# Kernel optimization log

Hardware: AMD Instinct MI355X
Metric: run time of the kernel (lower is better)

Reference implementation:

```python
import jax, jax.numpy as jnp
import numpy as np
import math
jax.config.update("jax_enable_x64", True)

# dims matching init_kwargs
BS, N_IND, N_STEP, ORDER = 32, 8, 100, 2
N_ORD = ORDER + 1            # number of derivative orders tracked (y, y', y'')
N_IV, N_IV_STEPS = 2, 1
NVAR = N_STEP * N_ORD        # qp variables per ODE (eps column is dropped: A[..., 1:])
DT = jnp.float64             # solver_dbl=True


def _static_parts():
    # initial-value constraint rows: u[t, j] = iv_rhs for t < n_iv_steps, j < n_iv
    iv_rows = N_IV_STEPS * N_IV
    Iv = np.zeros((iv_rows, NVAR))
    r = 0
    for t in range(N_IV_STEPS):
        for j in range(N_IV):
            Iv[r, t * N_ORD + j] = 1.0
            r += 1
    # Taylor expansion tables: fact[i, j] = 1/(j-i)! for j>=i else 0; expn[i,j] = j-i
    i_idx = np.arange(ORDER)[:, None]
    j_idx = np.arange(N_ORD)[None, :]
    dmask = j_idx >= i_idx
    d = np.where(dmask, j_idx - i_idx, 0)
    fact = np.where(dmask, 1.0 / np.array([[math.factorial(v) for v in row] for row in d]), 0.0)
    sign = np.where(dmask, (-1.0) ** d, 0.0)
    Imat = np.eye(ORDER, N_ORD)
    return (jnp.asarray(Iv, DT), jnp.asarray(fact, DT), jnp.asarray(d, DT),
            jnp.asarray(sign, DT), jnp.asarray(Imat, DT))


def _solve(coeffs, rhs, iv_rhs, steps):
    # coeffs: (B, n_step, n_ord), rhs: (B, n_step), iv_rhs: (B, iv_rows), steps: (B, n_step-1)
    B = coeffs.shape[0]
    T1 = N_STEP - 1
    R = 2 * ORDER + 1  # fwd Taylor rows (ORDER) + bwd Taylor rows (ORDER) + central row (1)
    Iv, fact, expn, sign, Imat = _static_parts()

    # equation constraints: block-diagonal in step: sum_j coeffs[b,t,j] * u[t,j] = rhs[b,t]
    eye = jnp.eye(N_STEP, dtype=DT)
    Eq = jnp.einsum('ts,bsj->btsj', eye, coeffs).reshape(B, N_STEP, NVAR)
    IvB = jnp.broadcast_to(Iv[None], (B,) + Iv.shape)

    # smoothness constraints per interval t -> t+1 with step h = steps[b,t]
    h = steps[:, :, None, None]                  # (B, T1, 1, 1)
    hp = h ** expn                               # h^(j-i)
    fwd_t = fact * hp                            # fwd Taylor: sum_j h^(j-i)/(j-i)! u[t,j] - u[t+1,i] = 0
    bwd_t1 = fact * sign * hp                    # bwd Taylor: sum_j (-h)^(j-i)/(j-i)! u[t+1,j] - u[t,i] = 0
    ImB = jnp.broadcast_to(Imat, fwd_t.shape)
    hh = steps[:, :, None]                       # (B, T1, 1)
    e_m1 = jnp.zeros((N_ORD,), DT).at[ORDER - 1].set(1.0)
    e_o = jnp.zeros((N_ORD,), DT).at[ORDER].set(1.0)
    # central (trapezoid) rule on highest derivative:
    # u[t+1,ord-1] - u[t,ord-1] - h/2 (u[t,ord] + u[t+1,ord]) = 0
    ct = -e_m1 - 0.5 * hh * e_o                  # (B, T1, n_ord) coeffs on block t
    ct1 = e_m1 - 0.5 * hh * e_o                  # coeffs on block t+1
    Dt = jnp.concatenate([fwd_t, -ImB, ct[:, :, None, :]], axis=2)    # (B,T1,R,n_ord)
    Dt1 = jnp.concatenate([-ImB, bwd_t1, ct1[:, :, None, :]], axis=2)

    Dfull = jnp.zeros((B, T1, R, N_STEP, N_ORD), DT)
    t = jnp.arange(T1)
    Dfull = Dfull.at[:, t, :, t, :].set(jnp.moveaxis(Dt, 1, 0))
    Dfull = Dfull.at[:, t, :, t + 1, :].set(jnp.moveaxis(Dt1, 1, 0))
    D = Dfull.reshape(B, T1 * R, NVAR)

    A = jnp.concatenate([Eq, IvB, D], axis=1)    # dense AG (eps column dropped)
    beta = jnp.concatenate([rhs, iv_rhs, jnp.zeros((B, T1 * R), DT)], axis=1)

    AtA = jnp.einsum('bmi,bmj->bij', A, A)
    Atb = jnp.einsum('bmi,bm->bi', A, beta)
    L = jnp.linalg.cholesky(AtA)
    x = jax.scipy.linalg.cho_solve((L, True), Atb[..., None])[..., 0]
    return x


def setup_inputs() -> dict:
    key = jax.random.key(0)
    k1, k2, k3, k4 = jax.random.split(key, 4)
    coeffs = jax.random.normal(k1, (BS, N_IND, N_STEP, N_ORD), dtype=jnp.float32)
    rhs = jax.random.normal(k2, (BS, N_IND, N_STEP), dtype=jnp.float32)
    iv_rhs = jax.random.normal(k3, (BS, N_IND, N_IV_STEPS * N_IV), dtype=jnp.float32)
    # positive step sizes around the module's step_size=0.1
    steps = 0.05 + 0.1 * jax.random.uniform(k4, (BS, N_IND, N_STEP - 1), dtype=jnp.float32)
    return {"coeffs": coeffs, "rhs": rhs, "iv_rhs": iv_rhs, "steps": steps}


def reference(coeffs, rhs, iv_rhs, steps):
    B = BS * N_IND
    c = coeffs.reshape(B, N_STEP, N_ORD).astype(DT)   # n_dim = 1 folded in
    r = rhs.reshape(B, N_STEP).astype(DT)
    iv = iv_rhs.reshape(B, N_IV_STEPS * N_IV).astype(DT)
    st = steps.reshape(B, N_STEP - 1).astype(DT)
    x = _solve(c, r, iv, st)
    u = x.reshape(BS, N_IND, N_STEP, N_ORD)
    u0, u1, u2 = u[..., 0], u[..., 1], u[..., 2]
    eps = jnp.zeros((B,), DT)
    return (u0, u1, u2, eps, st[:, :, None])
```

## Files before the change

### kernel.cpp

```cpp
#include <hip/hip_runtime.h>

#define NPROB 256
#define NSTEP 100
#define T1    99

__device__ __forceinline__ void syminv3(const float A[6], float G[6]) {
    const float k00 = A[3] * A[5] - A[4] * A[4];
    const float k01 = A[2] * A[4] - A[1] * A[5];
    const float k02 = A[1] * A[4] - A[2] * A[3];
    const float det = A[0] * k00 + A[1] * k01 + A[2] * k02;
    const float id  = 1.0f / det;
    G[0] = k00 * id;
    G[1] = k01 * id;
    G[2] = k02 * id;
    G[3] = (A[0] * A[5] - A[2] * A[2]) * id;
    G[4] = (A[2] * A[1] - A[0] * A[4]) * id;
    G[5] = (A[0] * A[3] - A[1] * A[1]) * id;
}

__device__ __forceinline__ void symmul(const float G[6], const float M[9], float R[9]) {
#pragma unroll
    for (int c = 0; c < 3; ++c) {
        R[0 + c] = G[0] * M[c] + G[1] * M[3 + c] + G[2] * M[6 + c];
        R[3 + c] = G[1] * M[c] + G[3] * M[3 + c] + G[4] * M[6 + c];
        R[6 + c] = G[2] * M[c] + G[4] * M[3 + c] + G[5] * M[6 + c];
    }
}

__device__ __forceinline__ void symvec(const float G[6], const float v[3], float r[3]) {
    r[0] = G[0] * v[0] + G[1] * v[1] + G[2] * v[2];
    r[1] = G[1] * v[0] + G[3] * v[1] + G[4] * v[2];
    r[2] = G[2] * v[0] + G[4] * v[1] + G[5] * v[2];
}

__device__ __forceinline__ void pqz(const float A[6], const float C[9],
                                    const float B[9], const float b[3], float pub[21]) {
    float G[6];
    syminv3(A, G);
    symmul(G, C, pub);
    symmul(G, B, pub + 9);
    symvec(G, b, pub + 18);
}

__device__ __forceinline__ void upd(float A[6], float C[9], float B[9], float b[3],
                                    const float SL[21], const float SR[21]) {
    const float* Pl = SL;      const float* Ql = SL + 9;  const float* zl = SL + 18;
    const float* Pr = SR;      const float* Qr = SR + 9;  const float* zr = SR + 18;

    const int RI[6] = {0, 0, 0, 1, 1, 2};
    const int CI[6] = {0, 1, 2, 1, 2, 2};
#pragma unroll
    for (int e = 0; e < 6; ++e) {
        const int r = RI[e], c = CI[e];
        A[e] -= C[3 * r] * Ql[c] + C[3 * r + 1] * Ql[3 + c] + C[3 * r + 2] * Ql[6 + c]
              + B[3 * r] * Pr[c] + B[3 * r + 1] * Pr[3 + c] + B[3 * r + 2] * Pr[6 + c];
    }
    float nC[9], nB[9];
#pragma unroll
    for (int r = 0; r < 3; ++r)
#pragma unroll
        for (int c = 0; c < 3; ++c) {
            nC[3 * r + c] = -(C[3 * r] * Pl[c] + C[3 * r + 1] * Pl[3 + c] + C[3 * r + 2] * Pl[6 + c]);
            nB[3 * r + c] = -(B[3 * r] * Qr[c] + B[3 * r + 1] * Qr[3 + c] + B[3 * r + 2] * Qr[6 + c]);
        }
#pragma unroll
    for (int r = 0; r < 3; ++r)
        b[r] -= C[3 * r] * zl[0] + C[3 * r + 1] * zl[1] + C[3 * r + 2] * zl[2]
              + B[3 * r] * zr[0] + B[3 * r + 1] * zr[1] + B[3 * r + 2] * zr[2];
#pragma unroll
    for (int k = 0; k < 9; ++k) { C[k] = nC[k]; B[k] = nB[k]; }
}

__device__ __forceinline__ void build_row(int t, const float* cb, const float* rb,
                                          const float* sb, const float* ivp,
                                          float A[6], float C[9], float B[9], float b[3]) {
    const float c0 = cb[t * 3 + 0];
    const float c1 = cb[t * 3 + 1];
    const float c2 = cb[t * 3 + 2];
    const float r  = rb[t];
    A[0] = c0 * c0; A[1] = c0 * c1; A[2] = c0 * c2;
    A[3] = c1 * c1; A[4] = c1 * c2; A[5] = c2 * c2;
    b[0] = c0 * r;  b[1] = c1 * r;  b[2] = c2 * r;
#pragma unroll
    for (int k = 0; k < 9; ++k) { C[k] = 0.0f; B[k] = 0.0f; }

    if (t == 0) {
        A[0] += 1.0f; A[3] += 1.0f;
        b[0] += ivp[0];
        b[1] += ivp[1];
    }
    if (t < T1) {
        const float h = sb[t], h2 = h * h;
        A[0] += 2.0f;
        A[1] += h;
        A[2] += 0.5f * h2;
        A[3] += h2 + 3.0f;
        A[4] += 0.5f * h2 * h + 1.5f * h;
        A[5] += 0.25f * h2 * h2 + 1.25f * h2;
        B[0] = -2.0f;      B[1] =  h;        B[2] = -0.5f * h2;
        B[3] = -h;         B[4] = -3.0f;     B[5] =  1.5f * h;
        B[6] = -0.5f * h2; B[7] = -1.5f * h; B[8] =  0.25f * h2;
    }
    if (t > 0) {
        const float hm = sb[t - 1], hm2 = hm * hm;
        A[0] += 2.0f;
        A[1] -= hm;
        A[2] += 0.5f * hm2;
        A[3] += hm2 + 3.0f;
        A[4] -= 0.5f * hm2 * hm + 1.5f * hm;
        A[5] += 0.25f * hm2 * hm2 + 1.25f * hm2;
        C[0] = -2.0f;      C[1] = -hm;       C[2] = -0.5f * hm2;
        C[3] =  hm;        C[4] = -3.0f;     C[5] = -1.5f * hm;
        C[6] = -0.5f * hm2; C[7] = 1.5f * hm; C[8] = 0.25f * hm2;
    }
}

__device__ __forceinline__ void shflup21(const float v[21], float o[21], int s) {
#pragma unroll
    for (int k = 0; k < 21; ++k) o[k] = __shfl_up(v[k], s, 64);
}
__device__ __forceinline__ void shfldn21(const float v[21], float o[21], int s) {
#pragma unroll
    for (int k = 0; k < 21; ++k) o[k] = __shfl_down(v[k], s, 64);
}

__global__ __launch_bounds__(64, 1) void ode_pcr_shfl_kernel(
    const float* __restrict__ coeffs,
    const float* __restrict__ rhs,
    const float* __restrict__ iv_rhs,
    const float* __restrict__ steps,
    float* __restrict__ out)
{
    const int b = blockIdx.x;
    const int L = threadIdx.x;
    const bool act = (L < 50);

    const float* cb  = coeffs + b * NSTEP * 3;
    const float* rb  = rhs    + b * NSTEP;
    const float* sb  = steps  + b * T1;
    const float* ivp = iv_rhs + b * 2;

    float Ae[6], Ce[9], Be[9], be[3];
    float pubo[21];
#pragma unroll
    for (int k = 0; k < 21; ++k) pubo[k] = 0.0f;
#pragma unroll
    for (int k = 0; k < 6; ++k) Ae[k] = 0.0f;
#pragma unroll
    for (int k = 0; k < 9; ++k) { Ce[k] = 0.0f; Be[k] = 0.0f; }
    be[0] = be[1] = be[2] = 0.0f;

    if (act) {
        build_row(2 * L, cb, rb, sb, ivp, Ae, Ce, Be, be);
        float Ao[6], Co[9], Bo[9], bo[3];
        build_row(2 * L + 1, cb, rb, sb, ivp, Ao, Co, Bo, bo);
        pqz(Ao, Co, Bo, bo, pubo);
    }
    {
        float SL[21];
        shflup21(pubo, SL, 1);
        if (act) upd(Ae, Ce, Be, be, SL, pubo);
    }

#pragma unroll
    for (int lv = 0; lv < 6; ++lv) {
        const int s = 1 << lv;
        float pub[21];
#pragma unroll
        for (int k = 0; k < 21; ++k) pub[k] = 0.0f;
        if (act) pqz(Ae, Ce, Be, be, pub);
        float SL[21], SR[21];
        shflup21(pub, SL, s);
        shfldn21(pub, SR, s);
        if (act) upd(Ae, Ce, Be, be, SL, SR);
    }

    float xe[3] = {0.0f, 0.0f, 0.0f};
    if (act) {
        float G[6];
        syminv3(Ae, G);
        symvec(G, be, xe);
    }
    float xr[3];
    xr[0] = __shfl_down(xe[0], 1, 64);
    xr[1] = __shfl_down(xe[1], 1, 64);
    xr[2] = __shfl_down(xe[2], 1, 64);

    if (act) {
        const float* Po = pubo;
        const float* Qo = pubo + 9;
        const float* zo = pubo + 18;
        float xo[3];
#pragma unroll
        for (int r = 0; r < 3; ++r)
            xo[r] = zo[r]
                  - (Po[3 * r] * xe[0] + Po[3 * r + 1] * xe[1] + Po[3 * r + 2] * xe[2])
                  - (Qo[3 * r] * xr[0] + Qo[3 * r + 1] * xr[1] + Qo[3 * r + 2] * xr[2]);

        const int t0 = 2 * L, t1 = 2 * L + 1;
        out[            b * NSTEP + t0] = xe[0];
        out[            b * NSTEP + t1] = xo[0];
        out[25600 +     b * NSTEP + t0] = xe[1];
        out[25600 +     b * NSTEP + t1] = xo[1];
        out[51200 +     b * NSTEP + t0] = xe[2];
        out[51200 +     b * NSTEP + t1] = xo[2];
    }

    for (int t = L; t < T1; t += 64)
        out[77056 + b * T1 + t] = sb[t];
    if (L == 0)
        out[76800 + b] = 0.0f;
}

extern "C" void kernel_launch(void* const* d_in, const int* in_sizes, int n_in,
                              void* d_out, int out_size, void* d_ws, size_t ws_size,
                              hipStream_t stream) {
    const float* coeffs = (const float*)d_in[0];
    const float* rhs    = (const float*)d_in[1];
    const float* iv_rhs = (const float*)d_in[2];
    const float* steps  = (const float*)d_in[3];
    float* out = (float*)d_out;

    ode_pcr_shfl_kernel<<<dim3(NPROB), dim3(64), 0, stream>>>(
        coeffs, rhs, iv_rhs, steps, out);
}
```

Measured before the change: 65.05 us.

## Exploit block-tridiagonal symmetry in PCR to cut shuffles and matmuls

Reformulates the parallel cyclic reduction to use the symmetry of the normal-equation matrix (C = B^T of the previous row). Only the super-diagonal block is kept, and each lane exchanges compact symmetric products (W, y, G, z, Q) with its neighbours instead of full 21-float P/Q/z packets. The Q shuffle and the B update are also skipped on the final level. The goal is fewer cross-lane shuffles and less arithmetic per reduction level, at the cost of more intricate bookkeeping and possible changes in floating-point rounding.

```diff
diff --git a/kernel.cpp b/kernel.cpp
--- a/kernel.cpp
+++ b/kernel.cpp
@@ -27,53 +27,62 @@
     }
 }
 
+__device__ __forceinline__ void mulsym(const float M[9], const float G[6], float R[9]) {
+#pragma unroll
+    for (int r = 0; r < 3; ++r) {
+        R[3 * r + 0] = M[3 * r + 0] * G[0] + M[3 * r + 1] * G[1] + M[3 * r + 2] * G[2];
+        R[3 * r + 1] = M[3 * r + 0] * G[1] + M[3 * r + 1] * G[3] + M[3 * r + 2] * G[4];
+        R[3 * r + 2] = M[3 * r + 0] * G[2] + M[3 * r + 1] * G[4] + M[3 * r + 2] * G[5];
+    }
+}
+
 __device__ __forceinline__ void symvec(const float G[6], const float v[3], float r[3]) {
     r[0] = G[0] * v[0] + G[1] * v[1] + G[2] * v[2];
     r[1] = G[1] * v[0] + G[3] * v[1] + G[4] * v[2];
     r[2] = G[2] * v[0] + G[4] * v[1] + G[5] * v[2];
 }
 
-__device__ __forceinline__ void pqz(const float A[6], const float C[9],
-                                    const float B[9], const float b[3], float pub[21]) {
-    float G[6];
-    syminv3(A, G);
-    symmul(G, C, pub);
-    symmul(G, B, pub + 9);
-    symvec(G, b, pub + 18);
-}
-
-__device__ __forceinline__ void upd(float A[6], float C[9], float B[9], float b[3],
-                                    const float SL[21], const float SR[21]) {
-    const float* Pl = SL;      const float* Ql = SL + 9;  const float* zl = SL + 18;
-    const float* Pr = SR;      const float* Qr = SR + 9;  const float* zr = SR + 18;
-
-    const int RI[6] = {0, 0, 0, 1, 1, 2};
-    const int CI[6] = {0, 1, 2, 1, 2, 2};
-#pragma unroll
-    for (int e = 0; e < 6; ++e) {
-        const int r = RI[e], c = CI[e];
-        A[e] -= C[3 * r] * Ql[c] + C[3 * r + 1] * Ql[3 + c] + C[3 * r + 2] * Ql[6 + c]
-              + B[3 * r] * Pr[c] + B[3 * r + 1] * Pr[3 + c] + B[3 * r + 2] * Pr[6 + c];
-    }
-    float nC[9], nB[9];
+__device__ __forceinline__ void tvec(const float B[9], const float v[3], float r[3]) {
+#pragma unroll
+    for (int c = 0; c < 3; ++c)
+        r[c] = B[c] * v[0] + B[3 + c] * v[1] + B[6 + c] * v[2];
+}
+
+__device__ __forceinline__ void mvec(const float B[9], const float v[3], float r[3]) {
+#pragma unroll
+    for (int rr = 0; rr < 3; ++rr)
+        r[rr] = B[3 * rr] * v[0] + B[3 * rr + 1] * v[1] + B[3 * rr + 2] * v[2];
+}
+
+__device__ __forceinline__ void nmatmul(const float X[9], const float Y[9], float R[9]) {
 #pragma unroll
     for (int r = 0; r < 3; ++r)
 #pragma unroll
-        for (int c = 0; c < 3; ++c) {
-            nC[3 * r + c] = -(C[3 * r] * Pl[c] + C[3 * r + 1] * Pl[3 + c] + C[3 * r + 2] * Pl[6 + c]);
-            nB[3 * r + c] = -(B[3 * r] * Qr[c] + B[3 * r + 1] * Qr[3 + c] + B[3 * r + 2] * Qr[6 + c]);
-        }
-#pragma unroll
-    for (int r = 0; r < 3; ++r)
-        b[r] -= C[3 * r] * zl[0] + C[3 * r + 1] * zl[1] + C[3 * r + 2] * zl[2]
-              + B[3 * r] * zr[0] + B[3 * r + 1] * zr[1] + B[3 * r + 2] * zr[2];
-#pragma unroll
-    for (int k = 0; k < 9; ++k) { C[k] = nC[k]; B[k] = nB[k]; }
-}
-
-__device__ __forceinline__ void build_row(int t, const float* cb, const float* rb,
+        for (int c = 0; c < 3; ++c)
+            R[3 * r + c] = -(X[3 * r] * Y[c] + X[3 * r + 1] * Y[3 + c] + X[3 * r + 2] * Y[6 + c]);
+}
+
+__device__ __forceinline__ void mulbt_sym(const float M[9], const float B[9], float U[6]) {
+    U[0] = M[0] * B[0] + M[1] * B[1] + M[2] * B[2];
+    U[1] = M[0] * B[3] + M[1] * B[4] + M[2] * B[5];
+    U[2] = M[0] * B[6] + M[1] * B[7] + M[2] * B[8];
+    U[3] = M[3] * B[3] + M[4] * B[4] + M[5] * B[5];
+    U[4] = M[3] * B[6] + M[4] * B[7] + M[5] * B[8];
+    U[5] = M[6] * B[6] + M[7] * B[7] + M[8] * B[8];
+}
+
+__device__ __forceinline__ void btq_sym(const float B[9], const float Q[9], float W[6]) {
+    W[0] = B[0] * Q[0] + B[3] * Q[3] + B[6] * Q[6];
+    W[1] = B[0] * Q[1] + B[3] * Q[4] + B[6] * Q[7];
+    W[2] = B[0] * Q[2] + B[3] * Q[5] + B[6] * Q[8];
+    W[3] = B[1] * Q[1] + B[4] * Q[4] + B[7] * Q[7];
+    W[4] = B[1] * Q[2] + B[4] * Q[5] + B[7] * Q[8];
+    W[5] = B[2] * Q[2] + B[5] * Q[5] + B[8] * Q[8];
+}
+
+__device__ __forceinline__ void build_sym(int t, const float* cb, const float* rb,
                                           const float* sb, const float* ivp,
-                                          float A[6], float C[9], float B[9], float b[3]) {
+                                          float A[6], float B[9], float b[3]) {
     const float c0 = cb[t * 3 + 0];
     const float c1 = cb[t * 3 + 1];
     const float c2 = cb[t * 3 + 2];
@@ -82,7 +91,7 @@
     A[3] = c1 * c1; A[4] = c1 * c2; A[5] = c2 * c2;
     b[0] = c0 * r;  b[1] = c1 * r;  b[2] = c2 * r;
 #pragma unroll
-    for (int k = 0; k < 9; ++k) { C[k] = 0.0f; B[k] = 0.0f; }
+    for (int k = 0; k < 9; ++k) B[k] = 0.0f;
 
     if (t == 0) {
         A[0] += 1.0f; A[3] += 1.0f;
@@ -109,22 +118,21 @@
         A[3] += hm2 + 3.0f;
         A[4] -= 0.5f * hm2 * hm + 1.5f * hm;
         A[5] += 0.25f * hm2 * hm2 + 1.25f * hm2;
-        C[0] = -2.0f;      C[1] = -hm;       C[2] = -0.5f * hm2;
-        C[3] =  hm;        C[4] = -3.0f;     C[5] = -1.5f * hm;
-        C[6] = -0.5f * hm2; C[7] = 1.5f * hm; C[8] = 0.25f * hm2;
-    }
-}
-
-__device__ __forceinline__ void shflup21(const float v[21], float o[21], int s) {
-#pragma unroll
-    for (int k = 0; k < 21; ++k) o[k] = __shfl_up(v[k], s, 64);
-}
-__device__ __forceinline__ void shfldn21(const float v[21], float o[21], int s) {
-#pragma unroll
-    for (int k = 0; k < 21; ++k) o[k] = __shfl_down(v[k], s, 64);
-}
-
-__global__ __launch_bounds__(64, 1) void ode_pcr_shfl_kernel(
+    }
+}
+
+template <int N>
+__device__ __forceinline__ void shup(const float* v, float* o, int s) {
+#pragma unroll
+    for (int k = 0; k < N; ++k) o[k] = __shfl_up(v[k], s, 64);
+}
+template <int N>
+__device__ __forceinline__ void shdn(const float* v, float* o, int s) {
+#pragma unroll
+    for (int k = 0; k < N; ++k) o[k] = __shfl_down(v[k], s, 64);
+}
+
+__global__ __launch_bounds__(64, 1) void ode_pcr_sym_kernel(
     const float* __restrict__ coeffs,
     const float* __restrict__ rhs,
     const float* __restrict__ iv_rhs,
@@ -140,39 +148,103 @@
     const float* sb  = steps  + b * T1;
     const float* ivp = iv_rhs + b * 2;
 
-    float Ae[6], Ce[9], Be[9], be[3];
-    float pubo[21];
-#pragma unroll
-    for (int k = 0; k < 21; ++k) pubo[k] = 0.0f;
-#pragma unroll
-    for (int k = 0; k < 6; ++k) Ae[k] = 0.0f;
-#pragma unroll
-    for (int k = 0; k < 9; ++k) { Ce[k] = 0.0f; Be[k] = 0.0f; }
+    float Ae[6], Be[9], be[3];
+    float Po[9], Qo[9], zo[3];
+    float Wp[6], yp[3];
+#pragma unroll
+    for (int k = 0; k < 6; ++k) { Ae[k] = 0.0f; Wp[k] = 0.0f; }
+#pragma unroll
+    for (int k = 0; k < 9; ++k) { Be[k] = 0.0f; Po[k] = 0.0f; Qo[k] = 0.0f; }
     be[0] = be[1] = be[2] = 0.0f;
+    zo[0] = zo[1] = zo[2] = 0.0f;
+    yp[0] = yp[1] = yp[2] = 0.0f;
+
+    float U[6], Bn[9], bz[3];
 
     if (act) {
-        build_row(2 * L, cb, rb, sb, ivp, Ae, Ce, Be, be);
-        float Ao[6], Co[9], Bo[9], bo[3];
-        build_row(2 * L + 1, cb, rb, sb, ivp, Ao, Co, Bo, bo);
-        pqz(Ao, Co, Bo, bo, pubo);
+        build_sym(2 * L, cb, rb, sb, ivp, Ae, Be, be);
+        float Ao[6], Bo[9], bo[3];
+        build_sym(2 * L + 1, cb, rb, sb, ivp, Ao, Bo, bo);
+
+        float G[6];
+        syminv3(Ao, G);
+        symmul(G, Bo, Qo);
+        symvec(G, bo, zo);
+        btq_sym(Bo, Qo, Wp);
+        tvec(Bo, zo, yp);
+
+        float M[9];
+        mulsym(Be, G, M);
+        Po[0] = M[0]; Po[1] = M[3]; Po[2] = M[6];
+        Po[3] = M[1]; Po[4] = M[4]; Po[5] = M[7];
+        Po[6] = M[2]; Po[7] = M[5]; Po[8] = M[8];
+        mulbt_sym(M, Be, U);
+        nmatmul(Be, Qo, Bn);
+        mvec(Be, zo, bz);
     }
     {
-        float SL[21];
-        shflup21(pubo, SL, 1);
-        if (act) upd(Ae, Ce, Be, be, SL, pubo);
+        float Wl[6], yl[3];
+        shup<6>(Wp, Wl, 1);
+        shup<3>(yp, yl, 1);
+        if (act) {
+#pragma unroll
+            for (int k = 0; k < 6; ++k) Wl[k] = (L > 0) ? Wl[k] : 0.0f;
+#pragma unroll
+            for (int k = 0; k < 3; ++k) yl[k] = (L > 0) ? yl[k] : 0.0f;
+#pragma unroll
+            for (int k = 0; k < 6; ++k) Ae[k] -= Wl[k] + U[k];
+#pragma unroll
+            for (int k = 0; k < 3; ++k) be[k] -= yl[k] + bz[k];
+#pragma unroll
+            for (int k = 0; k < 9; ++k) Be[k] = Bn[k];
+        }
     }
 
 #pragma unroll
     for (int lv = 0; lv < 6; ++lv) {
         const int s = 1 << lv;
-        float pub[21];
-#pragma unroll
-        for (int k = 0; k < 21; ++k) pub[k] = 0.0f;
-        if (act) pqz(Ae, Ce, Be, be, pub);
-        float SL[21], SR[21];
-        shflup21(pub, SL, s);
-        shfldn21(pub, SR, s);
-        if (act) upd(Ae, Ce, Be, be, SL, SR);
+        const bool last = (lv == 5);
+
+        float G[6] = {0, 0, 0, 0, 0, 0};
+        float Q[9] = {0, 0, 0, 0, 0, 0, 0, 0, 0};
+        float z[3] = {0, 0, 0};
+        float W[6] = {0, 0, 0, 0, 0, 0};
+        float y[3] = {0, 0, 0};
+        if (act) {
+            syminv3(Ae, G);
+            symmul(G, Be, Q);
+            symvec(G, be, z);
+            btq_sym(Be, Q, W);
+            tvec(Be, z, y);
+        }
+        float Wl[6], yl[3], Gr[6], zr[3], Qr[9];
+        shup<6>(W, Wl, s);
+        shup<3>(y, yl, s);
+        shdn<6>(G, Gr, s);
+        shdn<3>(z, zr, s);
+        if (!last) shdn<9>(Q, Qr, s);
+
+        if (act) {
+#pragma unroll
+            for (int k = 0; k < 6; ++k) Wl[k] = (L >= s) ? Wl[k] : 0.0f;
+#pragma unroll
+            for (int k = 0; k < 3; ++k) yl[k] = (L >= s) ? yl[k] : 0.0f;
+
+            float M[9];
+            mulsym(Be, Gr, M);
+            mulbt_sym(M, Be, U);
+            mvec(Be, zr, bz);
+            if (!last) nmatmul(Be, Qr, Bn);
+
+#pragma unroll
+            for (int k = 0; k < 6; ++k) Ae[k] -= Wl[k] + U[k];
+#pragma unroll
+            for (int k = 0; k < 3; ++k) be[k] -= yl[k] + bz[k];
+            if (!last) {
+#pragma unroll
+                for (int k = 0; k < 9; ++k) Be[k] = Bn[k];
+            }
+        }
     }
 
     float xe[3] = {0.0f, 0.0f, 0.0f};
@@ -187,9 +259,6 @@
     xr[2] = __shfl_down(xe[2], 1, 64);
 
     if (act) {
-        const float* Po = pubo;
-        const float* Qo = pubo + 9;
-        const float* zo = pubo + 18;
         float xo[3];
 #pragma unroll
         for (int r = 0; r < 3; ++r)
@@ -221,6 +290,6 @@
     const float* steps  = (const float*)d_in[3];
     float* out = (float*)d_out;
 
-    ode_pcr_shfl_kernel<<<dim3(NPROB), dim3(64), 0, stream>>>(
+    ode_pcr_sym_kernel<<<dim3(NPROB), dim3(64), 0, stream>>>(
         coeffs, rhs, iv_rhs, steps, out);
 }
```

After: 63.87 us. Within noise of the previous version (-1.8%).
